# Optimization experiments

Measured on AMD Instinct MI355X. Metric: run time of the kernel, lower is better.

The kernel has to match this reference:

```python
import jax, jax.numpy as jnp
import numpy as np

B, T, I, H, O = 8, 4096, 128, 256, 64
H2 = 2 * H  # bidirectional feature size


def _init(key, shape, scale):
    return (jax.random.uniform(key, shape, jnp.float32) * 2.0 - 1.0) * scale


def setup_inputs() -> dict:
    key = jax.random.key(0)
    ks = jax.random.split(key, 14)
    s = 1.0 / np.sqrt(H)  # torch GRU init scale
    return {
        "x": jax.random.normal(ks[0], (B, T, I), jnp.float32),
        # forward-direction GRU params (gate order: r, z, n)
        "w_ih_f": _init(ks[1], (3 * H, I), s),
        "w_hh_f": _init(ks[2], (3 * H, H), s),
        "b_ih_f": _init(ks[3], (3 * H,), s),
        "b_hh_f": _init(ks[4], (3 * H,), s),
        # backward-direction GRU params
        "w_ih_b": _init(ks[5], (3 * H, I), s),
        "w_hh_b": _init(ks[6], (3 * H, H), s),
        "b_ih_b": _init(ks[7], (3 * H,), s),
        "b_hh_b": _init(ks[8], (3 * H,), s),
        # attention params
        "w_att": jax.random.normal(ks[9], (H2, H2), jnp.float32) * (1.0 / np.sqrt(H2)),
        "v_att": jax.random.normal(ks[10], (H2, 1), jnp.float32) * (1.0 / np.sqrt(H2)),
        # output linear
        "w_lin": _init(ks[11], (O, H2), 1.0 / np.sqrt(H2)),
        "b_lin": _init(ks[12], (O,), 1.0 / np.sqrt(H2)),
    }


def _run_gru(x, w_ih, w_hh, b_ih, b_hh, reverse):
    # x: [B,T,I] -> outputs [B,T,H]. PyTorch GRU cell math, gates ordered r,z,n.
    gx = jnp.einsum("bti,gi->btg", x, w_ih) + b_ih  # precompute input gates [B,T,3H]
    gx = jnp.moveaxis(gx, 1, 0)  # [T,B,3H] for scan

    def step(h, gxt):
        gh = h @ w_hh.T + b_hh  # [B,3H]
        xr, xz, xn = jnp.split(gxt, 3, axis=-1)
        hr, hz, hn = jnp.split(gh, 3, axis=-1)
        r = jax.nn.sigmoid(xr + hr)
        z = jax.nn.sigmoid(xz + hz)
        n = jnp.tanh(xn + r * hn)
        h_new = (1.0 - z) * n + z * h
        return h_new, h_new

    h0 = jnp.zeros((x.shape[0], w_hh.shape[1]), x.dtype)
    _, hs = jax.lax.scan(step, h0, gx, reverse=reverse)  # outputs time-aligned
    return jnp.moveaxis(hs, 0, 1)  # [B,T,H]


def reference(x, w_ih_f, w_hh_f, b_ih_f, b_hh_f, w_ih_b, w_hh_b, b_ih_b, b_hh_b,
              w_att, v_att, w_lin, b_lin):
    hf = _run_gru(x, w_ih_f, w_hh_f, b_ih_f, b_hh_f, reverse=False)
    hb = _run_gru(x, w_ih_b, w_hh_b, b_ih_b, b_hh_b, reverse=True)
    pred = jnp.concatenate([hf, hb], axis=-1)  # [B,T,2H]
    # attention over time: fused replacement of per-timestep mm/cat loops
    squish = jnp.tanh(jnp.einsum("bth,hk->btk", pred, w_att))  # [B,T,2H]
    scores = jnp.einsum("btk,k->bt", squish, v_att[:, 0])  # [B,T]
    a = jax.nn.softmax(scores, axis=-1)  # [B,T]
    ctx = jnp.einsum("bt,bth->bh", a, pred)  # [B,2H]
    logits = ctx @ w_lin.T + b_lin  # [B,O]
    return jax.nn.softmax(logits, axis=-1)
```

## Files before the change

### kernel.cpp

```cpp
#include <hip/hip_runtime.h>
#include <cstdint>
#include <cstddef>

#define NB 8
#define NT 4096
#define NI 128
#define NH 256
#define NH2 512
#define NO 64
#define NSLICE 8
#define NJS 32

#define OFF_H64   0
#define OFF_MIR   16384
#define OFF_XCC   32768
#define OFF_SC    33024
#define OFF_CTX   65792
#define OFF_WT    69888
#define OFF_PRED  332032
#define ZERO_FLOATS 69888

__device__ __forceinline__ void st_plain(unsigned long long* p, unsigned long long v) {
    asm volatile("global_store_dwordx2 %0, %1, off" :: "v"(p), "v"(v) : "memory");
}
__device__ __forceinline__ unsigned long long ld_l2(const unsigned long long* p) {
    unsigned long long v;
    asm volatile("global_load_dwordx2 %0, %1, off sc0\n\ts_waitcnt vmcnt(0)"
                 : "=v"(v) : "v"(p) : "memory");
    return v;
}

__global__ __launch_bounds__(384, 1) void gru_rec(
    const float* __restrict__ x,
    const float* __restrict__ w_ih_f, const float* __restrict__ w_hh_f,
    const float* __restrict__ b_ih_f, const float* __restrict__ b_hh_f,
    const float* __restrict__ w_ih_b, const float* __restrict__ w_hh_b,
    const float* __restrict__ b_ih_b, const float* __restrict__ b_hh_b,
    unsigned long long* __restrict__ hbuf, unsigned long long* __restrict__ mir,
    unsigned long long* __restrict__ xccbuf, float* __restrict__ pred)
{
    const int wg = blockIdx.x;
    const int dir = wg & 1;
    const int bb = (wg >> 1) & 7;
    const int slice = wg >> 4;
    const int tid = threadIdx.x;
    const int row = tid >> 2;
    const int q = tid & 3;
    const int g = row >> 5;
    const int jj = row & 31;
    const int grow = g * NH + slice * NJS + jj;

    const float* wih = dir ? w_ih_b : w_ih_f;
    const float* whh = dir ? w_hh_b : w_hh_f;
    const float* bih = dir ? b_ih_b : b_ih_f;
    const float* bhh = dir ? b_hh_b : b_hh_f;

    float wh[64], wi[32];
    {
        const float* p = whh + (size_t)grow * NH + q * 64;
        #pragma unroll
        for (int i = 0; i < 16; ++i) {
            float4 v = *(const float4*)(p + i * 4);
            wh[4*i] = v.x; wh[4*i+1] = v.y; wh[4*i+2] = v.z; wh[4*i+3] = v.w;
        }
        const float* p2 = wih + (size_t)grow * NI + q * 32;
        #pragma unroll
        for (int i = 0; i < 8; ++i) {
            float4 v = *(const float4*)(p2 + i * 4);
            wi[4*i] = v.x; wi[4*i+1] = v.y; wi[4*i+2] = v.z; wi[4*i+3] = v.w;
        }
    }
    const float bi = bih[grow];
    const float bh = bhh[grow];

    __shared__ float h_lds[268];
    __shared__ float x_lds[140];
    __shared__ float gx_l[96], gh_l[96];
    __shared__ int fast_flag;

    if (tid == 0) {
        unsigned xcc;
        asm volatile("s_getreg_b32 %0, hwreg(HW_REG_XCC_ID)" : "=s"(xcc));
        xcc &= 0xFu;
        unsigned long long* xb64 = xccbuf + (size_t)(wg & 15) * NSLICE;
        __hip_atomic_store(&xb64[slice],
                           (1ull << 32) | (unsigned long long)xcc,
                           __ATOMIC_RELAXED, __HIP_MEMORY_SCOPE_AGENT);
        int same = 1;
        for (int p = 0; p < NSLICE; ++p) {
            unsigned long long pk;
            do {
                pk = __hip_atomic_load(&xb64[p], __ATOMIC_RELAXED,
                                       __HIP_MEMORY_SCOPE_AGENT);
            } while ((unsigned)(pk >> 32) != 1u);
            same &= ((unsigned)pk == xcc);
        }
        fast_flag = same;
    }
    __syncthreads();
    bool use_fast = (fast_flag != 0);

    unsigned long long* hb = hbuf + (size_t)(dir * NB + bb) * 2 * NH;
    unsigned long long* mb = mir  + (size_t)(dir * NB + bb) * 2 * NH;
    const float* xb = x + (size_t)bb * NT * NI;
    float* predb = pred + (size_t)bb * NT * NH2 + dir * NH;

    const int xc = tid - NH;
    float xreg = 0.f;
    if (tid >= NH) {
        const int t0 = dir ? (NT - 1) : 0;
        xreg = xb[(size_t)t0 * NI + xc];
    }

    for (int s = 0; s < NT; ++s) {
        const int t = dir ? (NT - 1 - s) : s;
        const int pr = s & 1, pw = pr ^ 1;

        if (tid < NH) {
            const unsigned tag = (unsigned)s;
            unsigned long long pk = 0;
            bool got = false;
            if (use_fast) {
                const unsigned long long* fp = hb + pr * NH + tid;
                #pragma unroll 1
                for (int tries = 0; tries < 8; ++tries) {
                    pk = ld_l2(fp);
                    if ((unsigned)(pk >> 32) == tag) { got = true; break; }
                }
                if (!got) use_fast = false;
            }
            if (!got) {
                const unsigned long long* mp = mb + pr * NH + tid;
                do {
                    pk = __hip_atomic_load(mp, __ATOMIC_RELAXED,
                                           __HIP_MEMORY_SCOPE_AGENT);
                } while ((unsigned)(pk >> 32) != tag);
            }
            h_lds[tid + 4 * (tid >> 6)] = __uint_as_float((unsigned)pk);
        } else {
            x_lds[xc + 4 * (xc >> 5)] = xreg;
        }
        __syncthreads();

        float ah = 0.f, ax = 0.f;
        {
            const float* hp = h_lds + q * 68;
            #pragma unroll
            for (int i = 0; i < 64; ++i) ah += wh[i] * hp[i];
            const float* xp = x_lds + q * 36;
            #pragma unroll
            for (int i = 0; i < 32; ++i) ax += wi[i] * xp[i];
        }
        ah += __shfl_xor(ah, 1); ah += __shfl_xor(ah, 2);
        ax += __shfl_xor(ax, 1); ax += __shfl_xor(ax, 2);
        if (q == 0) { gx_l[row] = ax + bi; gh_l[row] = ah + bh; }
        if (tid >= NH && s + 1 < NT) {
            const int tn = dir ? (NT - 2 - s) : (s + 1);
            xreg = xb[(size_t)tn * NI + xc];
        }
        __syncthreads();

        if (tid < NJS) {
            const float xr = gx_l[tid],      hr = gh_l[tid];
            const float xz = gx_l[32 + tid], hz = gh_l[32 + tid];
            const float xn = gx_l[64 + tid], hn = gh_l[64 + tid];
            const float r = 1.f / (1.f + __expf(-(xr + hr)));
            const float z = 1.f / (1.f + __expf(-(xz + hz)));
            const float y = xn + r * hn;
            const float e2 = __expf(-2.f * y);
            const float n = (1.f - e2) / (1.f + e2);
            const int c = slice * NJS + tid;
            const float hold = h_lds[c + 4 * (c >> 6)];
            const float hnew = (1.f - z) * n + z * hold;
            predb[(size_t)t * NH2 + c] = hnew;
            const unsigned long long pk =
                ((unsigned long long)(unsigned)(s + 1) << 32) |
                (unsigned long long)__float_as_uint(hnew);
            st_plain(hb + pw * NH + c, pk);
            __hip_atomic_store(mb + pw * NH + c, pk,
                               __ATOMIC_RELAXED, __HIP_MEMORY_SCOPE_AGENT);
        }
        __syncthreads();
    }
}

__global__ void transpose_watt(const float* __restrict__ w_att, float* __restrict__ wT) {
    const int n = blockIdx.x * 256 + threadIdx.x;
    const int k = n >> 9, h = n & 511;
    wT[n] = w_att[h * NH2 + k];
}

__global__ __launch_bounds__(256) void scores_gemm(
    const float* __restrict__ pred, const float* __restrict__ wT,
    const float* __restrict__ v_att, float* __restrict__ scores)
{
    const int tt = blockIdx.x, kt = blockIdx.y, bb = blockIdx.z;
    const int tid = threadIdx.x;
    const int tx = tid & 15;
    const int ty = tid >> 4;
    __shared__ float As[64][68];
    __shared__ float Bs[64][68];
    __shared__ float red[64][17];
    float acc[4][4] = {{0.f}};
    const int t0 = tt * 64, k0 = kt * 64;
    const float* pb = pred + ((size_t)bb * NT + t0) * NH2;

    for (int hc = 0; hc < NH2; hc += 64) {
        #pragma unroll
        for (int r = 0; r < 4; ++r) {
            const int idx = tid + 256 * r;
            const int tr = idx >> 4;
            const int c4 = (idx & 15) * 4;
            float4 a = *(const float4*)(pb + (size_t)tr * NH2 + hc + c4);
            *(float4*)&As[tr][c4] = a;
            float4 w = *(const float4*)(wT + (size_t)(k0 + tr) * NH2 + hc + c4);
            Bs[c4 + 0][tr] = w.x; Bs[c4 + 1][tr] = w.y;
            Bs[c4 + 2][tr] = w.z; Bs[c4 + 3][tr] = w.w;
        }
        __syncthreads();
        #pragma unroll
        for (int h = 0; h < 64; ++h) {
            const float a0 = As[ty*4+0][h], a1 = As[ty*4+1][h];
            const float a2 = As[ty*4+2][h], a3 = As[ty*4+3][h];
            const float4 bv = *(const float4*)&Bs[h][tx*4];
            acc[0][0] += a0*bv.x; acc[0][1] += a0*bv.y; acc[0][2] += a0*bv.z; acc[0][3] += a0*bv.w;
            acc[1][0] += a1*bv.x; acc[1][1] += a1*bv.y; acc[1][2] += a1*bv.z; acc[1][3] += a1*bv.w;
            acc[2][0] += a2*bv.x; acc[2][1] += a2*bv.y; acc[2][2] += a2*bv.z; acc[2][3] += a2*bv.w;
            acc[3][0] += a3*bv.x; acc[3][1] += a3*bv.y; acc[3][2] += a3*bv.z; acc[3][3] += a3*bv.w;
        }
        __syncthreads();
    }
    const float4 vv = *(const float4*)(v_att + k0 + tx * 4);
    #pragma unroll
    for (int i = 0; i < 4; ++i) {
        const float p = tanhf(acc[i][0]) * vv.x + tanhf(acc[i][1]) * vv.y
                      + tanhf(acc[i][2]) * vv.z + tanhf(acc[i][3]) * vv.w;
        red[ty*4+i][tx] = p;
    }
    __syncthreads();
    if (tid < 64) {
        float ssum = 0.f;
        #pragma unroll
        for (int xx = 0; xx < 16; ++xx) ssum += red[tid][xx];
        atomicAdd(&scores[bb * NT + t0 + tid], ssum);
    }
}

__global__ void softmax_t(float* __restrict__ scores) {
    const int bb = blockIdx.x;
    const int tid = threadIdx.x;
    __shared__ float red[256];
    float m = -1e30f;
    for (int t = tid; t < NT; t += 256) m = fmaxf(m, scores[bb*NT + t]);
    red[tid] = m; __syncthreads();
    for (int s2 = 128; s2; s2 >>= 1) { if (tid < s2) red[tid] = fmaxf(red[tid], red[tid+s2]); __syncthreads(); }
    m = red[0]; __syncthreads();
    float sum = 0.f;
    for (int t = tid; t < NT; t += 256) sum += expf(scores[bb*NT + t] - m);
    red[tid] = sum; __syncthreads();
    for (int s2 = 128; s2; s2 >>= 1) { if (tid < s2) red[tid] += red[tid+s2]; __syncthreads(); }
    const float inv = 1.f / red[0];
    for (int t = tid; t < NT; t += 256) scores[bb*NT + t] = expf(scores[bb*NT + t] - m) * inv;
}

__global__ void ctx_kernel(const float* __restrict__ pred, const float* __restrict__ a,
                           float* __restrict__ ctx) {
    const int bb = blockIdx.x, ch = blockIdx.y;
    const int tid = threadIdx.x;
    const int t0 = ch * 128;
    float acc0 = 0.f, acc1 = 0.f;
    for (int t = 0; t < 128; ++t) {
        const float av = a[bb*NT + t0 + t];
        const float* p = pred + ((size_t)bb * NT + t0 + t) * NH2;
        acc0 += av * p[tid];
        acc1 += av * p[tid + 256];
    }
    atomicAdd(&ctx[bb*NH2 + tid], acc0);
    atomicAdd(&ctx[bb*NH2 + tid + 256], acc1);
}

__global__ __launch_bounds__(512) void final_kernel(
    const float* __restrict__ ctx, const float* __restrict__ w_lin,
    const float* __restrict__ b_lin, float* __restrict__ out)
{
    const int tid = threadIdx.x;
    const int bb = tid >> 6, o = tid & 63;
    __shared__ float cl[NB][NH2];
    for (int i = tid; i < NB * NH2; i += 512) cl[i >> 9][i & 511] = ctx[i];
    __syncthreads();
    float acc = b_lin[o];
    for (int h = 0; h < NH2; h += 4) {
        const float4 w = *(const float4*)&w_lin[o * NH2 + h];
        acc += cl[bb][h]*w.x + cl[bb][h+1]*w.y + cl[bb][h+2]*w.z + cl[bb][h+3]*w.w;
    }
    float m = acc;
    for (int off = 32; off; off >>= 1) m = fmaxf(m, __shfl_xor(m, off));
    const float e = expf(acc - m);
    float ssum = e;
    for (int off = 32; off; off >>= 1) ssum += __shfl_xor(ssum, off);
    out[tid] = e / ssum;
}

extern "C" void kernel_launch(void* const* d_in, const int* in_sizes, int n_in,
                              void* d_out, int out_size, void* d_ws, size_t ws_size,
                              hipStream_t stream) {
    (void)in_sizes; (void)n_in; (void)out_size; (void)ws_size;
    const float* x      = (const float*)d_in[0];
    const float* w_ih_f = (const float*)d_in[1];
    const float* w_hh_f = (const float*)d_in[2];
    const float* b_ih_f = (const float*)d_in[3];
    const float* b_hh_f = (const float*)d_in[4];
    const float* w_ih_b = (const float*)d_in[5];
    const float* w_hh_b = (const float*)d_in[6];
    const float* b_ih_b = (const float*)d_in[7];
    const float* b_hh_b = (const float*)d_in[8];
    const float* w_att  = (const float*)d_in[9];
    const float* v_att  = (const float*)d_in[10];
    const float* w_lin  = (const float*)d_in[11];
    const float* b_lin  = (const float*)d_in[12];

    float* ws     = (float*)d_ws;
    unsigned long long* hbuf = (unsigned long long*)(ws + OFF_H64);
    unsigned long long* mir  = (unsigned long long*)(ws + OFF_MIR);
    unsigned long long* xcc  = (unsigned long long*)(ws + OFF_XCC);
    float* scores = ws + OFF_SC;
    float* ctx    = ws + OFF_CTX;
    float* wT     = ws + OFF_WT;
    float* pred   = ws + OFF_PRED;
    float* out    = (float*)d_out;

    hipMemsetAsync(d_ws, 0, (size_t)ZERO_FLOATS * sizeof(float), stream);
    hipLaunchKernelGGL(transpose_watt, dim3(1024), dim3(256), 0, stream, w_att, wT);
    hipLaunchKernelGGL(gru_rec, dim3(128), dim3(384), 0, stream,
                       x, w_ih_f, w_hh_f, b_ih_f, b_hh_f,
                       w_ih_b, w_hh_b, b_ih_b, b_hh_b, hbuf, mir, xcc, pred);
    hipLaunchKernelGGL(scores_gemm, dim3(64, 8, 8), dim3(256), 0, stream,
                       pred, wT, v_att, scores);
    hipLaunchKernelGGL(softmax_t, dim3(8), dim3(256), 0, stream, scores);
    hipLaunchKernelGGL(ctx_kernel, dim3(8, 32), dim3(256), 0, stream, pred, scores, ctx);
    hipLaunchKernelGGL(final_kernel, dim3(1), dim3(512), 0, stream, ctx, w_lin, b_lin, out);
}
```

Measured before the change: 6.135 ms.

## Group recurrence workgroups into teams by XCC and split dot-product accumulators

Each workgroup publishes its XCC id, and all 128 then compute a rank that groups workgroups on the same XCC into 8-member teams, each team owning one (direction, batch) recurrence. The goal is to let most teams use the fast L2-only handoff path instead of the slower agent-scope mirror. The fast-path retry limit is raised and early misses no longer disable it. The dot products are also split into several independent accumulators to shorten the dependency chain. The new mapping requires all 128 workgroups to be co-resident for the global exchange, and the extra retries can lengthen spins when a team spans XCCs.

Result: slower. 6.434 ms (+4.9%).

```diff
diff --git a/kernel.cpp b/kernel.cpp
--- a/kernel.cpp
+++ b/kernel.cpp
@@ -40,16 +40,59 @@
     unsigned long long* __restrict__ xccbuf, float* __restrict__ pred)
 {
     const int wg = blockIdx.x;
-    const int dir = wg & 1;
-    const int bb = (wg >> 1) & 7;
-    const int slice = wg >> 4;
     const int tid = threadIdx.x;
     const int row = tid >> 2;
     const int q = tid & 3;
     const int g = row >> 5;
     const int jj = row & 31;
+
+    __shared__ float h_lds[268];
+    __shared__ float x_lds[140];
+    __shared__ float gx_l[96], gh_l[96];
+    __shared__ unsigned short xcc_l[128];
+    __shared__ int s_team, s_slice, s_fast;
+
+    if (tid == 0) {
+        unsigned xcc;
+        asm volatile("s_getreg_b32 %0, hwreg(HW_REG_XCC_ID)" : "=s"(xcc));
+        xcc &= 0xFu;
+        __hip_atomic_store(&xccbuf[wg], (1ull << 32) | (unsigned long long)xcc,
+                           __ATOMIC_RELAXED, __HIP_MEMORY_SCOPE_AGENT);
+    }
+    if (tid < 128) {
+        unsigned long long pk;
+        do {
+            pk = __hip_atomic_load(&xccbuf[tid], __ATOMIC_RELAXED,
+                                   __HIP_MEMORY_SCOPE_AGENT);
+        } while ((unsigned)(pk >> 32) != 1u);
+        xcc_l[tid] = (unsigned short)(unsigned)pk;
+    }
+    __syncthreads();
+    if (tid == 0) {
+        int cnt[16];
+        for (int b2 = 0; b2 < 16; ++b2) cnt[b2] = 0;
+        for (int j = 0; j < 128; ++j) cnt[xcc_l[j]]++;
+        int pref[17]; pref[0] = 0;
+        for (int b2 = 0; b2 < 16; ++b2) pref[b2 + 1] = pref[b2] + cnt[b2];
+        const int myx = xcc_l[wg];
+        int within = 0;
+        for (int j = 0; j < wg; ++j) within += (xcc_l[j] == myx);
+        const int rank = pref[myx] + within;
+        const int team = rank >> 3;
+        const int lo = team * 8, hi = lo + 8;
+        int pure = 0;
+        for (int b2 = 0; b2 < 16; ++b2)
+            if (pref[b2] <= lo && hi <= pref[b2 + 1]) pure = 1;
+        s_team = team; s_slice = rank & 7; s_fast = pure;
+    }
+    __syncthreads();
+    const int team = s_team;
+    const int slice = s_slice;
+    const int dir = team & 1;
+    const int bb = team >> 1;
+    bool use_fast = (s_fast != 0);
+
     const int grow = g * NH + slice * NJS + jj;
-
     const float* wih = dir ? w_ih_b : w_ih_f;
     const float* whh = dir ? w_hh_b : w_hh_f;
     const float* bih = dir ? b_ih_b : b_ih_f;
@@ -73,35 +116,8 @@
     const float bi = bih[grow];
     const float bh = bhh[grow];
 
-    __shared__ float h_lds[268];
-    __shared__ float x_lds[140];
-    __shared__ float gx_l[96], gh_l[96];
-    __shared__ int fast_flag;
-
-    if (tid == 0) {
-        unsigned xcc;
-        asm volatile("s_getreg_b32 %0, hwreg(HW_REG_XCC_ID)" : "=s"(xcc));
-        xcc &= 0xFu;
-        unsigned long long* xb64 = xccbuf + (size_t)(wg & 15) * NSLICE;
-        __hip_atomic_store(&xb64[slice],
-                           (1ull << 32) | (unsigned long long)xcc,
-                           __ATOMIC_RELAXED, __HIP_MEMORY_SCOPE_AGENT);
-        int same = 1;
-        for (int p = 0; p < NSLICE; ++p) {
-            unsigned long long pk;
-            do {
-                pk = __hip_atomic_load(&xb64[p], __ATOMIC_RELAXED,
-                                       __HIP_MEMORY_SCOPE_AGENT);
-            } while ((unsigned)(pk >> 32) != 1u);
-            same &= ((unsigned)pk == xcc);
-        }
-        fast_flag = same;
-    }
-    __syncthreads();
-    bool use_fast = (fast_flag != 0);
-
-    unsigned long long* hb = hbuf + (size_t)(dir * NB + bb) * 2 * NH;
-    unsigned long long* mb = mir  + (size_t)(dir * NB + bb) * 2 * NH;
+    unsigned long long* hb = hbuf + (size_t)team * 2 * NH;
+    unsigned long long* mb = mir  + (size_t)team * 2 * NH;
     const float* xb = x + (size_t)bb * NT * NI;
     float* predb = pred + (size_t)bb * NT * NH2 + dir * NH;
 
@@ -123,11 +139,11 @@
             if (use_fast) {
                 const unsigned long long* fp = hb + pr * NH + tid;
                 #pragma unroll 1
-                for (int tries = 0; tries < 8; ++tries) {
+                for (int tries = 0; tries < 64; ++tries) {
                     pk = ld_l2(fp);
                     if ((unsigned)(pk >> 32) == tag) { got = true; break; }
                 }
-                if (!got) use_fast = false;
+                if (!got && s >= 16) use_fast = false;
             }
             if (!got) {
                 const unsigned long long* mp = mb + pr * NH + tid;
@@ -142,15 +158,26 @@
         }
         __syncthreads();
 
-        float ah = 0.f, ax = 0.f;
+        float ah0 = 0.f, ah1 = 0.f, ah2 = 0.f, ah3 = 0.f;
+        float ax0 = 0.f, ax1 = 0.f;
         {
             const float* hp = h_lds + q * 68;
             #pragma unroll
-            for (int i = 0; i < 64; ++i) ah += wh[i] * hp[i];
+            for (int i = 0; i < 16; ++i) {
+                ah0 += wh[i]      * hp[i];
+                ah1 += wh[16 + i] * hp[16 + i];
+                ah2 += wh[32 + i] * hp[32 + i];
+                ah3 += wh[48 + i] * hp[48 + i];
+            }
             const float* xp = x_lds + q * 36;
             #pragma unroll
-            for (int i = 0; i < 32; ++i) ax += wi[i] * xp[i];
-        }
+            for (int i = 0; i < 16; ++i) {
+                ax0 += wi[i]      * xp[i];
+                ax1 += wi[16 + i] * xp[16 + i];
+            }
+        }
+        float ah = (ah0 + ah1) + (ah2 + ah3);
+        float ax = ax0 + ax1;
         ah += __shfl_xor(ah, 1); ah += __shfl_xor(ah, 2);
         ax += __shfl_xor(ax, 1); ax += __shfl_xor(ax, 2);
         if (q == 0) { gx_l[row] = ax + bi; gh_l[row] = ah + bh; }
```
